# Optimization experiments

Measured on AMD Instinct MI355X. Metric: run time of the kernel, lower is better.

Reference implementation:

```python
import jax, jax.numpy as jnp
import numpy as np

DIM = 1024
RANK = 8
POOL = 16
SCALE = 8.0 / 8.0  # alpha / rank


def setup_inputs() -> dict:
    key = jax.random.key(0)
    ks = jax.random.split(key, 8)
    B, N = 8, 4096
    x = jax.random.normal(ks[0], (B, N, DIM), dtype=jnp.float32)
    weight = jax.random.normal(ks[1], (3 * DIM, DIM), dtype=jnp.float32) * 0.02
    bias = jax.random.normal(ks[2], (3 * DIM,), dtype=jnp.float32) * 0.02
    A_q_pool = jax.random.normal(ks[3], (POOL, DIM, RANK), dtype=jnp.float32) * 0.02
    B_q_pool = jax.random.normal(ks[4], (POOL, RANK, DIM), dtype=jnp.float32) * 0.02
    A_v_pool = jax.random.normal(ks[5], (POOL, DIM, RANK), dtype=jnp.float32) * 0.02
    B_v_pool = jax.random.normal(ks[6], (POOL, RANK, DIM), dtype=jnp.float32) * 0.02
    idx = jax.random.randint(ks[7], (B, 1), 0, POOL, dtype=jnp.int64 if jax.config.jax_enable_x64 else jnp.int32)
    frozen_mask = jnp.zeros((POOL,), dtype=bool)
    return {"x": x, "weight": weight, "bias": bias,
            "A_q_pool": A_q_pool, "B_q_pool": B_q_pool,
            "A_v_pool": A_v_pool, "B_v_pool": B_v_pool,
            "idx": idx, "frozen_mask": frozen_mask}


def _maybe_freeze(pool, i, fz):
    g = pool[i]  # [B, ., .] per-sample gather
    return jnp.where(fz, jax.lax.stop_gradient(g), g)


def reference(x, weight, bias, A_q_pool, B_q_pool, A_v_pool, B_v_pool, idx, frozen_mask):
    # Base QKV projection: [B, N, 3*dim]
    qkv = jnp.einsum('bni,oi->bno', x, weight) + bias
    i = idx[:, 0]                      # [B]
    fz = frozen_mask[i][:, None, None]  # [B,1,1]
    A_q = _maybe_freeze(A_q_pool, i, fz)  # [B, dim, rank]
    B_q = _maybe_freeze(B_q_pool, i, fz)  # [B, rank, dim]
    A_v = _maybe_freeze(A_v_pool, i, fz)
    B_v = _maybe_freeze(B_v_pool, i, fz)
    # Low-rank update: (x @ A) @ B, rank-8 bottleneck
    new_q = jnp.einsum('bnr,brj->bnj', jnp.einsum('bni,bir->bnr', x, A_q), B_q)
    new_v = jnp.einsum('bnr,brj->bnj', jnp.einsum('bni,bir->bnr', x, A_v), B_v)
    qkv = qkv.at[:, :, :DIM].add(SCALE * new_q)
    qkv = qkv.at[:, :, -DIM:].add(SCALE * new_v)
    return qkv
```

## Files before the change

kernel.cpp:

```cpp
#include <hip/hip_runtime.h>
#include <hip/hip_bf16.h>
#include <stdint.h>

#define DIM   1024
#define ODIM  3072
#define MROWS 32768
#define RANK  8

typedef unsigned short u16;
typedef __attribute__((ext_vector_type(8))) short short8;
typedef __attribute__((ext_vector_type(8))) unsigned short u16x8;
typedef __attribute__((ext_vector_type(4))) unsigned short u16x4;
typedef __attribute__((ext_vector_type(4))) float f32x4;

__device__ __forceinline__ u16 f2bf(float f) {
    uint32_t u = __float_as_uint(f);
    u += 0x7fffu + ((u >> 16) & 1u);
    return (u16)(u >> 16);
}

__device__ __forceinline__ void gl2lds16(const void* g, void* l) {
    __builtin_amdgcn_global_load_lds(
        (const __attribute__((address_space(1))) void*)(uintptr_t)g,
        (__attribute__((address_space(3))) void*)(uint32_t)(uintptr_t)l,
        16, 0, 0);
}

#define BAR()    do { asm volatile("" ::: "memory"); __builtin_amdgcn_s_barrier(); asm volatile("" ::: "memory"); } while (0)
#define WAITV4() asm volatile("s_waitcnt vmcnt(4)" ::: "memory")
#define WAITV2() asm volatile("s_waitcnt vmcnt(2)" ::: "memory")
#define WAITV0() asm volatile("s_waitcnt vmcnt(0)" ::: "memory")
#define WAITL0() asm volatile("s_waitcnt lgkmcnt(0)" ::: "memory")
#define WAITL8() asm volatile("s_waitcnt lgkmcnt(8)" ::: "memory")
#define SCHED0() __builtin_amdgcn_sched_barrier(0)


__device__ __forceinline__ u16x8 cvt8_nt(const float* __restrict__ src) {
    f32x4 a = __builtin_nontemporal_load(reinterpret_cast<const f32x4*>(src));
    f32x4 b = __builtin_nontemporal_load(reinterpret_cast<const f32x4*>(src) + 1);
    u16x8 o;
    o[0] = f2bf(a[0]); o[1] = f2bf(a[1]); o[2] = f2bf(a[2]); o[3] = f2bf(a[3]);
    o[4] = f2bf(b[0]); o[5] = f2bf(b[1]); o[6] = f2bf(b[2]); o[7] = f2bf(b[3]);
    return o;
}

__global__ __launch_bounds__(256) void k_prep(const float* __restrict__ x,
                                              const float* __restrict__ W,
                                              const float* __restrict__ Aq_pool,
                                              const float* __restrict__ Bq_pool,
                                              const float* __restrict__ Av_pool,
                                              const float* __restrict__ Bv_pool,
                                              const int* __restrict__ idx,
                                              u16* __restrict__ Xc,
                                              u16* __restrict__ Wk,
                                              u16* __restrict__ Wmq,
                                              u16* __restrict__ Wmv) {
    if (blockIdx.x < 2048) {
        const int stride = 2048 * 256;
        for (int t = blockIdx.x * 256 + threadIdx.x; t * 8 < MROWS * DIM; t += stride) {
            const int i = t * 8;
            *reinterpret_cast<u16x8*>(Xc + i) = cvt8_nt(x + i);
        }
        return;
    }
    if (blockIdx.x < 2560) {
        const int i = ((blockIdx.x - 2048) * 256 + threadIdx.x) * 8;
        *reinterpret_cast<u16x8*>(Wk + i) = cvt8_nt(W + (size_t)DIM * DIM + i);
        return;
    }
    const int bb = blockIdx.x - 2560;
    const int b  = bb >> 7;
    const int s  = (bb >> 6) & 1;
    const int og = bb & 63;
    const int p  = idx[b];
    const float* A  = (s ? Av_pool : Aq_pool) + (size_t)p * DIM * RANK;
    const float* Bp = (s ? Bv_pool : Bq_pool) + (size_t)p * RANK * DIM;
    const float* Ws = W + (size_t)(s ? 2048 : 0) * DIM;
    u16* dst = (s ? Wmv : Wmq) + (size_t)b * DIM * DIM;

    const int t  = threadIdx.x;
    const int i0 = t * 4;
    float a[4][8];
    #pragma unroll
    for (int ii = 0; ii < 4; ++ii) {
        float4 a0 = reinterpret_cast<const float4*>(A + (size_t)(i0 + ii) * RANK)[0];
        float4 a1 = reinterpret_cast<const float4*>(A + (size_t)(i0 + ii) * RANK)[1];
        a[ii][0] = a0.x; a[ii][1] = a0.y; a[ii][2] = a0.z; a[ii][3] = a0.w;
        a[ii][4] = a1.x; a[ii][5] = a1.y; a[ii][6] = a1.z; a[ii][7] = a1.w;
    }
    for (int r = 0; r < 16; ++r) {
        const int o = og * 16 + r;
        float bv[8];
        #pragma unroll
        for (int rr = 0; rr < 8; ++rr) bv[rr] = Bp[(size_t)rr * DIM + o];
        f32x4 w = __builtin_nontemporal_load(
            reinterpret_cast<const f32x4*>(Ws + (size_t)o * DIM + i0));
        u16x4 ov;
        #pragma unroll
        for (int ii = 0; ii < 4; ++ii) {
            float d = 0.f;
            #pragma unroll
            for (int rr = 0; rr < 8; ++rr) d += a[ii][rr] * bv[rr];
            ov[ii] = f2bf(w[ii] + d);
        }
        *reinterpret_cast<u16x4*>(dst + (size_t)o * DIM + i0) = ov;
    }
}


__device__ __forceinline__ void stage_half(const u16* __restrict__ mat, int row0, int tk,
                                           u16* dst, int wave, int lane) {
    const int lrow = lane >> 3;
    const int g    = (lane & 7) ^ lrow;
    const u16* gp = mat + (size_t)(row0 + wave * 8 + lrow) * DIM + tk + g * 8;
    u16* lp = dst + wave * 8 * 64;
    gl2lds16(gp, lp);
    gl2lds16(gp + (size_t)64 * DIM, lp + 64 * 64);
}

__device__ __forceinline__ void ds_read_A(const u16* sA, int wr, int lane,
                                          int kx0, int kx1, int mh, short8 (&a)[4][2]) {
    #pragma unroll
    for (int f = 0; f < 4; ++f) {
        const int row = wr * 64 + f * 16 + mh * 128 + (lane & 15);
        a[f][0] = *reinterpret_cast<const short8*>(sA + row * 64 + kx0);
        a[f][1] = *reinterpret_cast<const short8*>(sA + row * 64 + kx1);
    }
}
__device__ __forceinline__ void ds_read_B(const u16* sB, int wc, int lane,
                                          int kx0, int kx1, int nh, short8 (&b)[2][2]) {
    #pragma unroll
    for (int f = 0; f < 2; ++f) {
        const int row = wc * 16 + (nh * 2 + f) * 64 + (lane & 15);
        b[f][0] = *reinterpret_cast<const short8*>(sB + row * 64 + kx0);
        b[f][1] = *reinterpret_cast<const short8*>(sB + row * 64 + kx1);
    }
}

template <int MH, int NH>
__device__ __forceinline__ void mfma_quad(const short8 (&a)[4][2], const short8 (&b)[2][2],
                                          f32x4 (&acc)[8][4]) {
    #pragma unroll
    for (int ks = 0; ks < 2; ++ks)
        #pragma unroll
        for (int f = 0; f < 4; ++f)
            #pragma unroll
            for (int g = 0; g < 2; ++g)
                acc[MH * 4 + f][NH * 2 + g] = __builtin_amdgcn_mfma_f32_16x16x32_bf16(
                    a[f][ks], b[g][ks], acc[MH * 4 + f][NH * 2 + g], 0, 0, 0);
}

#define MFMA_BLOCK(MH, NH, AREG, BREG)                  \
    do {                                                \
        BAR();                                          \
        WAITL0();                                       \
        SCHED0();                                       \
        __builtin_amdgcn_s_setprio(1);                  \
        mfma_quad<MH, NH>(AREG, BREG, acc);             \
        __builtin_amdgcn_s_setprio(0);                  \
        SCHED0();                                       \
    } while (0)

__global__ __launch_bounds__(512, 2) void k_gemm(const u16* __restrict__ Xc,
                                                 const u16* __restrict__ Wk,
                                                 const u16* __restrict__ Wmq,
                                                 const u16* __restrict__ Wmv,
                                                 const float* __restrict__ bias,
                                                 float* __restrict__ out) {
    extern __shared__ u16 lds[];
    const int tid  = threadIdx.x;
    const int lane = tid & 63, wave = tid >> 6;
    const int wr = wave >> 2, wc = wave & 3;

    const int orig = blockIdx.x;
    const int wg   = (orig & 7) * 192 + (orig >> 3);
    const int bn   = wg % 12;
    const int bm   = wg / 12;
    const int m0 = bm * 256, n0 = bn * 256;
    const int batch = m0 >> 12;

    const u16* Bmat;
    int nc;
    if (n0 < DIM)           { Bmat = Wmq + (size_t)batch * DIM * DIM; nc = n0; }
    else if (n0 < 2 * DIM)  { Bmat = Wk;                              nc = n0 - DIM; }
    else                    { Bmat = Wmv + (size_t)batch * DIM * DIM; nc = n0 - 2 * DIM; }

    const int kx0 = (((lane >> 4)    ) ^ (lane & 7)) * 8;
    const int kx1 = (((lane >> 4) + 4) ^ (lane & 7)) * 8;

    f32x4 acc[8][4] = {};

    stage_half(Xc,   m0,       0, lds,                    wave, lane);
    stage_half(Bmat, nc,       0, lds + 16384,            wave, lane);
    stage_half(Bmat, nc + 128, 0, lds + 16384 + 128 * 64, wave, lane);
    stage_half(Xc,   m0 + 128, 0, lds + 128 * 64,         wave, lane);
    WAITV0(); BAR();

    #pragma unroll 1
    for (int t = 0; t < 15; ++t) {
        const u16* sA = lds + (t & 1) * 32768;
        const u16* sB = sA + 16384;
        u16* wA = lds + ((t + 1) & 1) * 32768;
        u16* wB = wA + 16384;
        const int tk1 = (t + 1) * 64;
        short8 a_lo[4][2], a_hi[4][2], b0[2][2], b1[2][2];

        ds_read_A(sA, wr, lane, kx0, kx1, 0, a_lo);
        ds_read_B(sB, wc, lane, kx0, kx1, 0, b0);
        stage_half(Xc, m0, tk1, wA, wave, lane);
        WAITL8();
        MFMA_BLOCK(0, 0, a_lo, b0);
        WAITV4(); BAR();

        ds_read_B(sB, wc, lane, kx0, kx1, 1, b1);
        stage_half(Bmat, nc, tk1, wB, wave, lane);
        MFMA_BLOCK(0, 1, a_lo, b1);
        WAITV4(); BAR();

        ds_read_A(sA, wr, lane, kx0, kx1, 1, a_hi);
        stage_half(Bmat, nc + 128, tk1, wB + 128 * 64, wave, lane);
        MFMA_BLOCK(1, 0, a_hi, b0);
        BAR();

        stage_half(Xc, m0 + 128, tk1, wA + 128 * 64, wave, lane);
        MFMA_BLOCK(1, 1, a_hi, b1);
        WAITV4(); BAR();
    }

    {
        const u16* sA = lds + 32768;
        const u16* sB = sA + 16384;
        short8 a_lo[4][2], a_hi[4][2], b0[2][2], b1[2][2];

        ds_read_A(sA, wr, lane, kx0, kx1, 0, a_lo);
        ds_read_B(sB, wc, lane, kx0, kx1, 0, b0);
        WAITL8();
        MFMA_BLOCK(0, 0, a_lo, b0);
        WAITV2(); BAR();

        ds_read_B(sB, wc, lane, kx0, kx1, 1, b1);
        MFMA_BLOCK(0, 1, a_lo, b1);
        WAITV0(); BAR();

        ds_read_A(sA, wr, lane, kx0, kx1, 1, a_hi);
        MFMA_BLOCK(1, 0, a_hi, b0);
        BAR();

        MFMA_BLOCK(1, 1, a_hi, b1);
    }

    const int cn = wc * 16 + (lane & 15);
    float bcol[4];
    #pragma unroll
    for (int ni = 0; ni < 4; ++ni) bcol[ni] = bias[n0 + cn + ni * 64];
    #pragma unroll
    for (int mi = 0; mi < 8; ++mi) {
        const int rb = m0 + wr * 64 + (mi & 3) * 16 + (mi >> 2) * 128 + (lane >> 4) * 4;
        #pragma unroll
        for (int v = 0; v < 4; ++v) {
            const size_t row = (size_t)(rb + v);
            #pragma unroll
            for (int ni = 0; ni < 4; ++ni)
                out[row * ODIM + (size_t)(n0 + cn + ni * 64)] = acc[mi][ni][v] + bcol[ni];
        }
    }
}

extern "C" void kernel_launch(void* const* d_in, const int* in_sizes, int n_in,
                              void* d_out, int out_size, void* d_ws, size_t ws_size,
                              hipStream_t stream) {
    const float* x      = (const float*)d_in[0];
    const float* weight = (const float*)d_in[1];
    const float* bias   = (const float*)d_in[2];
    const float* Aq     = (const float*)d_in[3];
    const float* Bq     = (const float*)d_in[4];
    const float* Av     = (const float*)d_in[5];
    const float* Bv     = (const float*)d_in[6];
    const int*   idx    = (const int*)d_in[7];
    float* out = (float*)d_out;

    u16* Xc  = (u16*)d_ws;
    u16* Wk  = Xc + (size_t)MROWS * DIM;
    u16* Wmq = Wk + (size_t)DIM * DIM;
    u16* Wmv = Wmq + (size_t)8 * DIM * DIM;

    hipFuncSetAttribute(reinterpret_cast<const void*>(k_gemm),
                        hipFuncAttributeMaxDynamicSharedMemorySize, 131072);

    k_prep<<<3584, 256, 0, stream>>>(x, weight, Aq, Bq, Av, Bv, idx, Xc, Wk, Wmq, Wmv);
    k_gemm<<<1536, 512, 131072, stream>>>(Xc, Wk, Wmq, Wmv, bias, out);
}
```

Measured before the change: 278.5 us.

## Load GEMM B operand directly to registers, stage only A in LDS

The weight (B) tile is no longer staged through shared memory. Each wave now loads its B fragments straight from global memory into registers, prefetching the next k-step between MFMA groups. Only the X (A) tile stays double-buffered in LDS, which halves dynamic shared memory from 128 KB to 64 KB and may allow two workgroups per CU. The cost is that waves with the same column index fetch identical B data redundantly through the cache. Strided global loads and a full vmcnt(0) wait plus barrier each iteration may also expose load latency.

```diff
diff --git a/kernel.cpp b/kernel.cpp
--- a/kernel.cpp
+++ b/kernel.cpp
@@ -27,13 +27,9 @@
 }
 
 #define BAR()    do { asm volatile("" ::: "memory"); __builtin_amdgcn_s_barrier(); asm volatile("" ::: "memory"); } while (0)
-#define WAITV4() asm volatile("s_waitcnt vmcnt(4)" ::: "memory")
-#define WAITV2() asm volatile("s_waitcnt vmcnt(2)" ::: "memory")
 #define WAITV0() asm volatile("s_waitcnt vmcnt(0)" ::: "memory")
 #define WAITL0() asm volatile("s_waitcnt lgkmcnt(0)" ::: "memory")
-#define WAITL8() asm volatile("s_waitcnt lgkmcnt(8)" ::: "memory")
 #define SCHED0() __builtin_amdgcn_sched_barrier(0)
-
 
 __device__ __forceinline__ u16x8 cvt8_nt(const float* __restrict__ src) {
     f32x4 a = __builtin_nontemporal_load(reinterpret_cast<const f32x4*>(src));
@@ -127,14 +123,15 @@
         a[f][1] = *reinterpret_cast<const short8*>(sA + row * 64 + kx1);
     }
 }
-__device__ __forceinline__ void ds_read_B(const u16* sB, int wc, int lane,
-                                          int kx0, int kx1, int nh, short8 (&b)[2][2]) {
-    #pragma unroll
-    for (int f = 0; f < 2; ++f) {
-        const int row = wc * 16 + (nh * 2 + f) * 64 + (lane & 15);
-        b[f][0] = *reinterpret_cast<const short8*>(sB + row * 64 + kx0);
-        b[f][1] = *reinterpret_cast<const short8*>(sB + row * 64 + kx1);
-    }
+
+__device__ __forceinline__ void load_B(const u16* __restrict__ bgl, int nh, int tk,
+                                       short8 (&b)[2][2]) {
+    #pragma unroll
+    for (int g = 0; g < 2; ++g)
+        #pragma unroll
+        for (int ks = 0; ks < 2; ++ks)
+            b[g][ks] = *reinterpret_cast<const short8*>(
+                bgl + (size_t)((nh * 2 + g) * 64) * DIM + tk + ks * 32);
 }
 
 template <int MH, int NH>
@@ -149,17 +146,6 @@
                 acc[MH * 4 + f][NH * 2 + g] = __builtin_amdgcn_mfma_f32_16x16x32_bf16(
                     a[f][ks], b[g][ks], acc[MH * 4 + f][NH * 2 + g], 0, 0, 0);
 }
-
-#define MFMA_BLOCK(MH, NH, AREG, BREG)                  \
-    do {                                                \
-        BAR();                                          \
-        WAITL0();                                       \
-        SCHED0();                                       \
-        __builtin_amdgcn_s_setprio(1);                  \
-        mfma_quad<MH, NH>(AREG, BREG, acc);             \
-        __builtin_amdgcn_s_setprio(0);                  \
-        SCHED0();                                       \
-    } while (0)
 
 __global__ __launch_bounds__(512, 2) void k_gemm(const u16* __restrict__ Xc,
                                                  const u16* __restrict__ Wk,
@@ -188,65 +174,63 @@
     const int kx0 = (((lane >> 4)    ) ^ (lane & 7)) * 8;
     const int kx1 = (((lane >> 4) + 4) ^ (lane & 7)) * 8;
 
+    const u16* bgl = Bmat + (size_t)(nc + wc * 16 + (lane & 15)) * DIM + (lane >> 4) * 8;
+
     f32x4 acc[8][4] = {};
-
-    stage_half(Xc,   m0,       0, lds,                    wave, lane);
-    stage_half(Bmat, nc,       0, lds + 16384,            wave, lane);
-    stage_half(Bmat, nc + 128, 0, lds + 16384 + 128 * 64, wave, lane);
-    stage_half(Xc,   m0 + 128, 0, lds + 128 * 64,         wave, lane);
+    short8 b0[2][2], b1[2][2];
+
+    stage_half(Xc, m0,       0, lds,            wave, lane);
+    stage_half(Xc, m0 + 128, 0, lds + 128 * 64, wave, lane);
+    load_B(bgl, 0, 0, b0);
+    load_B(bgl, 1, 0, b1);
     WAITV0(); BAR();
 
     #pragma unroll 1
     for (int t = 0; t < 15; ++t) {
-        const u16* sA = lds + (t & 1) * 32768;
-        const u16* sB = sA + 16384;
-        u16* wA = lds + ((t + 1) & 1) * 32768;
-        u16* wB = wA + 16384;
+        const u16* rbuf = lds + (t & 1) * 16384;
+        u16* wbuf = lds + ((t + 1) & 1) * 16384;
         const int tk1 = (t + 1) * 64;
-        short8 a_lo[4][2], a_hi[4][2], b0[2][2], b1[2][2];
-
-        ds_read_A(sA, wr, lane, kx0, kx1, 0, a_lo);
-        ds_read_B(sB, wc, lane, kx0, kx1, 0, b0);
-        stage_half(Xc, m0, tk1, wA, wave, lane);
-        WAITL8();
-        MFMA_BLOCK(0, 0, a_lo, b0);
-        WAITV4(); BAR();
-
-        ds_read_B(sB, wc, lane, kx0, kx1, 1, b1);
-        stage_half(Bmat, nc, tk1, wB, wave, lane);
-        MFMA_BLOCK(0, 1, a_lo, b1);
-        WAITV4(); BAR();
-
-        ds_read_A(sA, wr, lane, kx0, kx1, 1, a_hi);
-        stage_half(Bmat, nc + 128, tk1, wB + 128 * 64, wave, lane);
-        MFMA_BLOCK(1, 0, a_hi, b0);
-        BAR();
-
-        stage_half(Xc, m0 + 128, tk1, wA + 128 * 64, wave, lane);
-        MFMA_BLOCK(1, 1, a_hi, b1);
-        WAITV4(); BAR();
+        short8 a_lo[4][2], a_hi[4][2];
+
+        stage_half(Xc, m0,       tk1, wbuf,            wave, lane);
+        stage_half(Xc, m0 + 128, tk1, wbuf + 128 * 64, wave, lane);
+
+        ds_read_A(rbuf, wr, lane, kx0, kx1, 0, a_lo);
+        ds_read_A(rbuf, wr, lane, kx0, kx1, 1, a_hi);
+
+        WAITL0(); SCHED0();
+        __builtin_amdgcn_s_setprio(1);
+        mfma_quad<0, 0>(a_lo, b0, acc);
+        mfma_quad<1, 0>(a_hi, b0, acc);
+        __builtin_amdgcn_s_setprio(0);
+        SCHED0();
+
+        load_B(bgl, 0, tk1, b0);
+        SCHED0();
+
+        __builtin_amdgcn_s_setprio(1);
+        mfma_quad<0, 1>(a_lo, b1, acc);
+        mfma_quad<1, 1>(a_hi, b1, acc);
+        __builtin_amdgcn_s_setprio(0);
+        SCHED0();
+
+        load_B(bgl, 1, tk1, b1);
+
+        WAITV0(); BAR();
     }
 
     {
-        const u16* sA = lds + 32768;
-        const u16* sB = sA + 16384;
-        short8 a_lo[4][2], a_hi[4][2], b0[2][2], b1[2][2];
-
-        ds_read_A(sA, wr, lane, kx0, kx1, 0, a_lo);
-        ds_read_B(sB, wc, lane, kx0, kx1, 0, b0);
-        WAITL8();
-        MFMA_BLOCK(0, 0, a_lo, b0);
-        WAITV2(); BAR();
-
-        ds_read_B(sB, wc, lane, kx0, kx1, 1, b1);
-        MFMA_BLOCK(0, 1, a_lo, b1);
-        WAITV0(); BAR();
-
-        ds_read_A(sA, wr, lane, kx0, kx1, 1, a_hi);
-        MFMA_BLOCK(1, 0, a_hi, b0);
-        BAR();
-
-        MFMA_BLOCK(1, 1, a_hi, b1);
+        const u16* rbuf = lds + 16384;
+        short8 a_lo[4][2], a_hi[4][2];
+        ds_read_A(rbuf, wr, lane, kx0, kx1, 0, a_lo);
+        ds_read_A(rbuf, wr, lane, kx0, kx1, 1, a_hi);
+        WAITL0(); SCHED0();
+        __builtin_amdgcn_s_setprio(1);
+        mfma_quad<0, 0>(a_lo, b0, acc);
+        mfma_quad<1, 0>(a_hi, b0, acc);
+        mfma_quad<0, 1>(a_lo, b1, acc);
+        mfma_quad<1, 1>(a_hi, b1, acc);
+        __builtin_amdgcn_s_setprio(0);
     }
 
     const int cn = wc * 16 + (lane & 15);
@@ -285,8 +269,8 @@
     u16* Wmv = Wmq + (size_t)8 * DIM * DIM;
 
     hipFuncSetAttribute(reinterpret_cast<const void*>(k_gemm),
-                        hipFuncAttributeMaxDynamicSharedMemorySize, 131072);
+                        hipFuncAttributeMaxDynamicSharedMemorySize, 65536);
 
     k_prep<<<3584, 256, 0, stream>>>(x, weight, Aq, Bq, Av, Bv, idx, Xc, Wk, Wmq, Wmv);
-    k_gemm<<<1536, 512, 131072, stream>>>(Xc, Wk, Wmq, Wmv, bias, out);
-}
+    k_gemm<<<1536, 512, 65536, stream>>>(Xc, Wk, Wmq, Wmv, bias, out);
+}
```

After: 382.1 us. 37.2% more time.
